# Kernel tuning notes

Hardware: AMD Instinct MI355X
Metric: run time of the kernel (lower is better)

The kernel has to match this reference:

```python
import jax, jax.numpy as jnp
import numpy as np

N = 128000      # total nodes
B = 128         # graphs, 1000 nodes each
L = 4           # max_levels
S_MAX = 1000    # max cluster size (<= PositionalEncoding max_len)
H = 128         # hidden dim (all conv output dims equal)
IN_DIM = 128
OUT_DIM = 1
E = 1024000
TEMP = 0.1


def layer_norm(x, g, b, eps=1e-5):
    mu = jnp.mean(x, axis=-1, keepdims=True)
    v = jnp.mean((x - mu) ** 2, axis=-1, keepdims=True)
    return (x - mu) * jax.lax.rsqrt(v + eps) * g + b


def transformer_conv(x, src, dst, Wq, bq, Wk, bk, Wv, bv, Ws, bs):
    # PyG TransformerConv, heads=1: softmax over in-edges of each dst node
    q = x @ Wq + bq
    k = x @ Wk + bk
    v = x @ Wv + bv
    logits = jnp.sum(q[dst] * k[src], axis=-1) / jnp.sqrt(jnp.float32(q.shape[-1]))
    m = jax.ops.segment_max(logits, dst, num_segments=N)
    e = jnp.exp(logits - m[dst])
    s = jax.ops.segment_sum(e, dst, num_segments=N)
    alpha = e / s[dst]
    agg = jax.ops.segment_sum(alpha[:, None] * v[src], dst, num_segments=N)
    return agg + x @ Ws + bs  # root_weight skip connection


def pos_encoding(S, d):
    pos = jnp.arange(S, dtype=jnp.float32)[:, None]
    div = jnp.exp(jnp.arange(0, d, 2, dtype=jnp.float32) * (-jnp.log(10000.0) / d))
    pe = jnp.zeros((S, d), jnp.float32)
    pe = pe.at[:, 0::2].set(jnp.sin(pos * div))
    pe = pe.at[:, 1::2].set(jnp.cos(pos * div))
    return pe


def gru(xseq, Wih, Whh, bih, bhh):
    # xseq: [G, S, H] -> outputs [G, S, H]; torch GRU gate math
    G = xseq.shape[0]
    def step(h, x_t):
        gi = x_t @ Wih.T + bih
        gh = h @ Whh.T + bhh
        ir, iz, inn = jnp.split(gi, 3, axis=-1)
        hr, hz, hn = jnp.split(gh, 3, axis=-1)
        r = jax.nn.sigmoid(ir + hr)
        z = jax.nn.sigmoid(iz + hz)
        n = jnp.tanh(inn + r * hn)
        h_new = (1.0 - z) * n + z * h
        return h_new, h_new
    h0 = jnp.zeros((G, Whh.shape[1]), xseq.dtype)
    _, outs = jax.lax.scan(step, h0, jnp.swapaxes(xseq, 0, 1))
    return jnp.swapaxes(outs, 0, 1)


def _forward(x, tree_edge_index, call_sequences, batch,
             conv_Wq, conv_bq, conv_Wk, conv_bk, conv_Wv, conv_bv, conv_Ws, conv_bs,
             ln_g, ln_b, centers, proj_W, proj_b,
             gru_Wih, gru_Whh, gru_bih, gru_bhh, seqln_g, seqln_b,
             lin1_W, lin1_b, lin2_W, lin2_b):
    src, dst = tree_edge_index[0], tree_edge_index[1]
    h = x
    for i in range(3):  # conv1/bn1, conv2/bn2, conv4/bn4
        h = transformer_conv(h, src, dst, conv_Wq[i], conv_bq[i], conv_Wk[i],
                             conv_bk[i], conv_Wv[i], conv_bv[i], conv_Ws[i], conv_bs[i])
        h = jax.nn.relu(layer_norm(h, ln_g[i], ln_b[i]))

    # HierarchicalClassifier: cosine-sim soft assignment + center variance loss
    xn = h / jnp.maximum(jnp.linalg.norm(h, axis=-1, keepdims=True), 1e-8)
    cn = centers / jnp.maximum(jnp.linalg.norm(centers, axis=-1, keepdims=True), 1e-8)
    assign = jax.nn.softmax((xn @ cn.T) / TEMP, axis=-1)
    level_ids = jnp.argmax(assign, axis=1).astype(jnp.int32)
    iu0, iu1 = np.triu_indices(L, k=1)
    dvec = jnp.linalg.norm(centers[iu0] - centers[iu1], axis=-1)
    distance = -jnp.var(dvec, ddof=1)  # torch.var is unbiased

    # ragged gather + pad: group nodes by (graph, cluster), sort by call order
    G = B * L
    group = batch * L + level_ids                       # [N]
    order = jnp.argsort(group * N + call_sequences)     # sort by group, then call
    g_sorted = group[order]
    counts = jax.ops.segment_sum(jnp.ones((N,), jnp.int32), group, num_segments=G)
    starts = jnp.cumsum(counts) - counts
    pos = jnp.arange(N, dtype=jnp.int32) - starts[g_sorted]
    seq = jnp.zeros((G, S_MAX, H), h.dtype).at[g_sorted, pos].set(h[order])

    # SequentialRNN: proj -> pos-enc -> GRU -> LayerNorm -> ReLU (mask unused)
    sin = seq @ proj_W + proj_b + pos_encoding(S_MAX, H)[None]
    outs = gru(sin, gru_Wih, gru_Whh, gru_bih, gru_bhh)
    outs = jax.nn.relu(layer_norm(outs, seqln_g, seqln_b))

    # scatter valid positions back; singleton clusters keep raw features
    node_out = jnp.zeros_like(h).at[order].set(outs[g_sorted, pos])
    singleton = (counts[group] == 1)
    gout = jnp.where(singleton[:, None], h, node_out)

    y = jax.nn.gelu(gout @ lin1_W + lin1_b, approximate=False)
    y = jax.nn.sigmoid(y @ lin2_W + lin2_b)
    return y, distance


def setup_inputs():
    key = jax.random.key(0)
    ks = jax.random.split(key, 16)
    p = lambda k, s: jax.random.normal(k, s, jnp.float32) * 0.02
    return {
        "x": jax.random.normal(ks[0], (N, IN_DIM), jnp.float32),
        "tree_edge_index": jax.random.randint(ks[1], (2, E), 0, N, dtype=jnp.int32),
        "call_sequences": jax.random.permutation(ks[2], N).astype(jnp.int32),
        "batch": (jnp.arange(N, dtype=jnp.int32) * B) // N,  # 1000 nodes per graph
        "conv_Wq": p(ks[3], (3, H, H)), "conv_bq": jnp.zeros((3, H), jnp.float32),
        "conv_Wk": p(ks[4], (3, H, H)), "conv_bk": jnp.zeros((3, H), jnp.float32),
        "conv_Wv": p(ks[5], (3, H, H)), "conv_bv": jnp.zeros((3, H), jnp.float32),
        "conv_Ws": p(ks[6], (3, H, H)), "conv_bs": jnp.zeros((3, H), jnp.float32),
        "ln_g": jnp.ones((3, H), jnp.float32), "ln_b": jnp.zeros((3, H), jnp.float32),
        "centers": jax.random.normal(ks[7], (L, H), jnp.float32),
        "proj_W": p(ks[8], (H, H)), "proj_b": jnp.zeros((H,), jnp.float32),
        "gru_Wih": p(ks[9], (3 * H, H)), "gru_Whh": p(ks[10], (3 * H, H)),
        "gru_bih": jnp.zeros((3 * H,), jnp.float32), "gru_bhh": jnp.zeros((3 * H,), jnp.float32),
        "seqln_g": jnp.ones((H,), jnp.float32), "seqln_b": jnp.zeros((H,), jnp.float32),
        "lin1_W": p(ks[11], (H, 8)), "lin1_b": jnp.zeros((8,), jnp.float32),
        "lin2_W": p(ks[12], (8, OUT_DIM)), "lin2_b": jnp.zeros((OUT_DIM,), jnp.float32),
    }


def reference(x, tree_edge_index, call_sequences, batch,
              conv_Wq, conv_bq, conv_Wk, conv_bk, conv_Wv, conv_bv, conv_Ws, conv_bs,
              ln_g, ln_b, centers, proj_W, proj_b,
              gru_Wih, gru_Whh, gru_bih, gru_bhh, seqln_g, seqln_b,
              lin1_W, lin1_b, lin2_W, lin2_b):
    return _forward(x, tree_edge_index, call_sequences, batch,
                    conv_Wq, conv_bq, conv_Wk, conv_bk, conv_Wv, conv_bv, conv_Ws, conv_bs,
                    ln_g, ln_b, centers, proj_W, proj_b,
                    gru_Wih, gru_Whh, gru_bih, gru_bhh, seqln_g, seqln_b,
                    lin1_W, lin1_b, lin2_W, lin2_b)
```

## Files before the change

### kernel.cpp

```cpp
#include <hip/hip_runtime.h>

#define NN 128000
#define EE 1024000
#define HH 128
#define GG 512
#define SMAX 1000
#define NCHUNK 500

typedef unsigned int u32;
typedef unsigned short u16;

constexpr size_t NH     = (size_t)NN*HH;
constexpr size_t F_H    = 0;
constexpr size_t F_A    = NH;
constexpr size_t F_B    = 2*NH;
constexpr size_t F_NODE = F_A + (size_t)NN*192;
constexpr size_t F_CN   = 3*NH;
constexpr size_t F_WKT  = F_CN   + 512;
constexpr size_t F_WQK  = F_WKT  + 3*16384;
constexpr size_t F_BQK  = F_WQK  + 3*16384;
constexpr size_t F_CW   = F_BQK  + 3*128;
constexpr size_t F_PEW  = F_CW   + 128*384;
constexpr size_t F_PEB  = F_PEW  + 1000*384;
constexpr size_t F_END  = F_PEB  + 1000*128;

constexpr size_t I_ROWP = 0;
constexpr size_t I_CUR  = I_ROWP + NN + 8;
constexpr size_t I_COL  = I_CUR  + NN;
constexpr size_t I_GRP  = I_COL  + EE;
constexpr size_t I_INV  = I_GRP  + NN;
constexpr size_t I_POS  = I_INV  + NN;
constexpr size_t I_GN   = I_POS  + NN;
constexpr size_t I_CNT  = I_GN   + (size_t)GG*SMAX;
constexpr size_t I_CH   = I_CNT  + GG;
constexpr size_t I_BS   = I_CH   + (size_t)NCHUNK*GG;
constexpr size_t I_WT   = I_BS   + 512;
constexpr size_t I_END  = I_WT   + 64*384;

constexpr size_t WS_NEEDED = F_END*4 + I_END*4;

__device__ inline float wredf(float v){
  #pragma unroll
  for (int o = 32; o; o >>= 1) v += __shfl_xor(v, o);
  return v;
}
__device__ inline u32 bf16rne(float f){
  u32 u = __float_as_uint(f);
  return (u + 0x7fffu + ((u >> 16) & 1u)) >> 16;
}
__device__ inline float bf2f(u16 u){
  return __uint_as_float(((u32)u) << 16);
}
__device__ inline float frcp(float x){
#if __has_builtin(__builtin_amdgcn_rcpf)
  return __builtin_amdgcn_rcpf(x);
#else
  return 1.f / x;
#endif
}

typedef _Float16 h2_t __attribute__((ext_vector_type(2)));
__device__ inline float dot2f(u32 w, u32 h, float acc){
#if __has_builtin(__builtin_amdgcn_fdot2)
  return __builtin_amdgcn_fdot2(__builtin_bit_cast(h2_t, w),
                                __builtin_bit_cast(h2_t, h), acc, false);
#else
  float r;
  asm("v_dot2_f32_f16 %0, %1, %2, %3" : "=v"(r) : "v"(w), "v"(h), "v"(acc));
  return r;
#endif
}
#define PIN4(v) asm volatile("" : "+v"((v).x), "+v"((v).y), "+v"((v).z), "+v"((v).w))

__global__ void k_sentinel(float* __restrict__ out, int n, float val){
  int i = blockIdx.x * 256 + threadIdx.x;
  if (i < n) out[i] = val;
}

__global__ void k_zero(int* __restrict__ p){
  p[blockIdx.x * 256 + threadIdx.x] = 0;
}
__global__ void k_hist(const int* __restrict__ dst, int* __restrict__ deg){
  int e = blockIdx.x * 256 + threadIdx.x;
  atomicAdd(&deg[dst[e]], 1);
}
__global__ void k_s1(const int* __restrict__ deg, int* __restrict__ bsum){
  __shared__ int red[256];
  int t = threadIdx.x;
  red[t] = deg[blockIdx.x * 256 + t];
  __syncthreads();
  for (int s = 128; s; s >>= 1){ if (t < s) red[t] += red[t + s]; __syncthreads(); }
  if (!t) bsum[blockIdx.x] = red[0];
}
__global__ void k_s2(int* __restrict__ bsum){
  __shared__ int arr[512];
  int t = threadIdx.x;
  int v0 = (t < NCHUNK) ? bsum[t] : 0;
  arr[t] = v0; __syncthreads();
  for (int off = 1; off < 512; off <<= 1){
    int v = (t >= off) ? arr[t - off] : 0;
    __syncthreads();
    arr[t] += v;
    __syncthreads();
  }
  if (t < NCHUNK) bsum[t] = arr[t] - v0;
}
__global__ void k_s3(const int* __restrict__ bsum, int* __restrict__ row_ptr,
                     int* __restrict__ cursor){
  __shared__ int arr[256];
  int t = threadIdx.x;
  int i = blockIdx.x * 256 + t;
  int v0 = cursor[i];
  arr[t] = v0; __syncthreads();
  for (int off = 1; off < 256; off <<= 1){
    int v = (t >= off) ? arr[t - off] : 0;
    __syncthreads();
    arr[t] += v;
    __syncthreads();
  }
  int exc = arr[t] - v0 + bsum[blockIdx.x];
  row_ptr[i] = exc;
  cursor[i]  = exc;
  if (i == 0) row_ptr[NN] = EE;
}
__global__ void k_scatter(const int* __restrict__ src, const int* __restrict__ dst,
                          int* __restrict__ cursor, int* __restrict__ col){
  int e = blockIdx.x * 256 + threadIdx.x;
  int idx = atomicAdd(&cursor[dst[e]], 1);
  col[idx] = src[e];
}

__global__ void k_setup(const float* __restrict__ centers, float* __restrict__ cn,
                        float* __restrict__ dist_out){
  __shared__ float red[128];
  int t = threadIdx.x;
  for (int l = 0; l < 4; ++l){
    float v = centers[l*128 + t];
    red[t] = v * v; __syncthreads();
    for (int s = 64; s; s >>= 1){ if (t < s) red[t] += red[t + s]; __syncthreads(); }
    float nrm = sqrtf(red[0]);
    __syncthreads();
    cn[l*128 + t] = v / fmaxf(nrm, 1e-8f);
  }
  const int iu0[6] = {0,0,0,1,1,2}, iu1[6] = {1,2,3,2,3,3};
  __shared__ float dv[6];
  for (int p = 0; p < 6; ++p){
    float d = centers[iu0[p]*128 + t] - centers[iu1[p]*128 + t];
    red[t] = d * d; __syncthreads();
    for (int s = 64; s; s >>= 1){ if (t < s) red[t] += red[t + s]; __syncthreads(); }
    if (!t) dv[p] = sqrtf(red[0]);
    __syncthreads();
  }
  if (!t){
    float mean = 0.f;
    for (int p = 0; p < 6; ++p) mean += dv[p];
    mean /= 6.f;
    float var = 0.f;
    for (int p = 0; p < 6; ++p){ float d = dv[p] - mean; var += d * d; }
    var /= 5.f;
    dist_out[0] = -var;
  }
}

__global__ void k_pe(const float* __restrict__ projb, float* __restrict__ peb){
  int p = blockIdx.x, t = threadIdx.x;
  float ex  = (float)(t >> 1) * (-2.0f * 9.210340371976184f / 128.0f);
  float ang = (float)p * expf(ex);
  float v = (t & 1) ? cosf(ang) : sinf(ang);
  peb[p*128 + t] = v + projb[t];
}
__global__ void k_pew(const float* __restrict__ peb, const float* __restrict__ Wih,
                      const float* __restrict__ bih, float* __restrict__ pew){
  int p = blockIdx.x;
  int j = blockIdx.y * 128 + threadIdx.x;
  const float* pb = peb + p*128;
  const float* wr = Wih + (size_t)j*128;
  float acc = bih[j];
  #pragma unroll 4
  for (int m = 0; m < 128; ++m) acc += pb[m] * wr[m];
  pew[(size_t)p*384 + j] = acc;
}
__global__ void k_combw(const float* __restrict__ projW, const float* __restrict__ Wih,
                        float* __restrict__ cw){
  int kk = blockIdx.x;
  int j  = blockIdx.y * 128 + threadIdx.x;
  const float* pr = projW + (size_t)kk*128;
  const float* wr = Wih + (size_t)j*128;
  float acc = 0.f;
  #pragma unroll 4
  for (int m = 0; m < 128; ++m) acc += pr[m] * wr[m];
  cw[(size_t)kk*384 + j] = acc;
}
__global__ void k_tr(const float* __restrict__ Wk, float* __restrict__ wkt){
  int kk = blockIdx.x, l = blockIdx.y, c = threadIdx.x;
  wkt[(size_t)l*16384 + kk*128 + c] = Wk[(size_t)l*16384 + c*128 + kk];
}
__global__ void k_mv(const float* __restrict__ M, const float* __restrict__ v,
                     float* __restrict__ out){
  int l = blockIdx.x, i = threadIdx.x;
  const float* row = M + (size_t)l*16384 + (size_t)i*128;
  const float* vv = v + l*128;
  float acc = 0.f;
  #pragma unroll 4
  for (int j = 0; j < 128; ++j) acc += row[j] * vv[j];
  out[l*128 + i] = acc;
}
__global__ void k_packwhh16(const float* __restrict__ Whh, u32* __restrict__ wt){
  int kp = blockIdx.x;
  int j  = blockIdx.y * 128 + threadIdx.x;
  _Float16 a = (_Float16)Whh[(size_t)j*128 + 2*kp];
  _Float16 b = (_Float16)Whh[(size_t)j*128 + 2*kp + 1];
  u32 lo = (u32)__builtin_bit_cast(u16, a);
  u32 hi = (u32)__builtin_bit_cast(u16, b);
  wt[(size_t)j*64 + kp] = (hi << 16) | lo;
}

__global__ __launch_bounds__(256, 2) void k_gemm(
    const float* __restrict__ X, const float* __restrict__ W, int ldw,
    const float* __restrict__ X2, const float* __restrict__ W2,
    const float* __restrict__ bias, const float* __restrict__ pew,
    const int* __restrict__ pos, float* __restrict__ out,
    u16* __restrict__ outb, int ldo,
    const float* __restrict__ lng, const float* __restrict__ lnb,
    const float* __restrict__ bvv, const int* __restrict__ rowp){
  __shared__ __align__(16) float Wl[64*132];
  __shared__ __align__(16) float Xl[64*132];
  int tid = threadIdx.x;
  int rb = blockIdx.x * 128;
  int cb = blockIdx.y * 128;
  int rg = tid >> 4;
  int cg = tid & 15;
  int kxor = (cg >> 2) & 3;
  float acc[8][8];
  #pragma unroll
  for (int a = 0; a < 8; ++a)
    #pragma unroll
    for (int b = 0; b < 8; ++b) acc[a][b] = 0.f;
  int nhalf = X2 ? 4 : 2;
  for (int half = 0; half < nhalf; ++half){
    const float* Xs = (half < 2) ? X : X2;
    const float* Ws = (half < 2) ? W : W2;
    int ldws = (half < 2) ? ldw : 128;
    int hk = half & 1;
    __syncthreads();
    #pragma unroll
    for (int it = 0; it < 8; ++it){
      int idx = it*256 + tid;
      int kk = idx >> 5, c4 = idx & 31;
      *(float4*)&Wl[kk*132 + c4*4] =
          *(const float4*)&Ws[(size_t)(hk*64 + kk)*ldws + cb + c4*4];
    }
    #pragma unroll
    for (int it = 0; it < 8; ++it){
      int idx = it*256 + tid;
      int r = idx >> 4, c4 = idx & 15;
      float4 xv = *(const float4*)&Xs[(size_t)(rb + r)*128 + hk*64 + c4*4];
      Xl[(c4*4+0)*132 + r] = xv.x;
      Xl[(c4*4+1)*132 + r] = xv.y;
      Xl[(c4*4+2)*132 + r] = xv.z;
      Xl[(c4*4+3)*132 + r] = xv.w;
    }
    __syncthreads();
    #pragma unroll 2
    for (int kk = 0; kk < 64; ++kk){
      int kx = kk ^ kxor;
      float4 wa = *(const float4*)&Wl[kx*132 + cg*8];
      float4 wb = *(const float4*)&Wl[kx*132 + cg*8 + 4];
      float4 xa = *(const float4*)&Xl[kx*132 + rg*8];
      float4 xb = *(const float4*)&Xl[kx*132 + rg*8 + 4];
      float xs[8] = {xa.x, xa.y, xa.z, xa.w, xb.x, xb.y, xb.z, xb.w};
      float ws[8] = {wa.x, wa.y, wa.z, wa.w, wb.x, wb.y, wb.z, wb.w};
      #pragma unroll
      for (int rr = 0; rr < 8; ++rr)
        #pragma unroll
        for (int j = 0; j < 8; ++j) acc[rr][j] += xs[rr] * ws[j];
    }
  }
  if (lng){
    float gv[8], bl[8], bb[8], vv[8];
    #pragma unroll
    for (int j = 0; j < 8; ++j){
      int c = cg*8 + j;
      gv[j] = lng[c]; bl[j] = lnb[c]; bb[j] = bias[c]; vv[j] = bvv[c];
    }
    #pragma unroll
    for (int rr = 0; rr < 8; ++rr){
      int r = rb + rg*8 + rr;
      bool deg = rowp[r+1] > rowp[r];
      float rs = 0.f, rq = 0.f;
      #pragma unroll
      for (int j = 0; j < 8; ++j){
        float v = acc[rr][j] + bb[j] + (deg ? vv[j] : 0.f);
        acc[rr][j] = v;
        rs += v; rq += v*v;
      }
      #pragma unroll
      for (int o = 8; o; o >>= 1){ rs += __shfl_xor(rs, o); rq += __shfl_xor(rq, o); }
      float mu = rs * 0.0078125f;
      float var = rq * 0.0078125f - mu*mu;
      float rstd = rsqrtf(var + 1e-5f);
      float ov[8];
      #pragma unroll
      for (int j = 0; j < 8; ++j)
        ov[j] = fmaxf((acc[rr][j] - mu)*rstd*gv[j] + bl[j], 0.f);
      float* op = out + (size_t)r*128 + cg*8;
      *(float4*)op       = *(const float4*)&ov[0];
      *(float4*)(op + 4) = *(const float4*)&ov[4];
    }
    return;
  }
  #pragma unroll
  for (int rr = 0; rr < 8; ++rr){
    int r = rb + rg*8 + rr;
    float bv[8];
    if (pos){
      const float* pw = pew + (size_t)pos[r]*384 + cb + cg*8;
      #pragma unroll
      for (int j = 0; j < 8; ++j) bv[j] = pw[j];
    } else if (bias){
      #pragma unroll
      for (int j = 0; j < 8; ++j) bv[j] = bias[cb + cg*8 + j];
    } else {
      #pragma unroll
      for (int j = 0; j < 8; ++j) bv[j] = 0.f;
    }
    if (outb){
      u16 ob[8];
      #pragma unroll
      for (int j = 0; j < 8; ++j) ob[j] = (u16)bf16rne(acc[rr][j] + bv[j]);
      *(uint4*)(outb + (size_t)r*ldo + cb + cg*8) = *(const uint4*)ob;
    } else {
      float ov[8];
      #pragma unroll
      for (int j = 0; j < 8; ++j) ov[j] = acc[rr][j] + bv[j];
      float* op = out + (size_t)r*ldo + cb + cg*8;
      *(float4*)op       = *(const float4*)&ov[0];
      *(float4*)(op + 4) = *(const float4*)&ov[4];
    }
  }
}

__global__ __launch_bounds__(256) void k_edge(
    const float* __restrict__ qt, const float* __restrict__ xsrc,
    const int* __restrict__ row_ptr, const int* __restrict__ col,
    float* __restrict__ xagg){
  int d = blockIdx.x * 8 + (threadIdx.x >> 5);
  int lane = threadIdx.x & 31;
  int e0 = row_ptr[d], e1 = row_ptr[d+1];
  if (e0 == e1){
    *(float4*)&xagg[(size_t)d*128 + lane*4] = make_float4(0.f, 0.f, 0.f, 0.f);
    return;
  }
  const float S = 0.08838834764831845f;
  float4 qv = *(const float4*)&qt[(size_t)d*128 + lane*4];
  float ss0 = 0.f, ss1 = 0.f;
  float4 A0 = make_float4(0.f,0.f,0.f,0.f), A1 = make_float4(0.f,0.f,0.f,0.f);
  int e = e0;
  for (; e + 1 < e1; e += 2){
    float4 x0 = *(const float4*)&xsrc[(size_t)col[e]  *128 + lane*4];
    float4 x1 = *(const float4*)&xsrc[(size_t)col[e+1]*128 + lane*4];
    float p0 = qv.x*x0.x + qv.y*x0.y + qv.z*x0.z + qv.w*x0.w;
    float p1 = qv.x*x1.x + qv.y*x1.y + qv.z*x1.z + qv.w*x1.w;
    #pragma unroll
    for (int o = 16; o; o >>= 1){ p0 += __shfl_xor(p0, o); p1 += __shfl_xor(p1, o); }
    float el0 = __expf(p0 * S);
    float el1 = __expf(p1 * S);
    ss0 += el0; ss1 += el1;
    A0.x += el0*x0.x; A0.y += el0*x0.y; A0.z += el0*x0.z; A0.w += el0*x0.w;
    A1.x += el1*x1.x; A1.y += el1*x1.y; A1.z += el1*x1.z; A1.w += el1*x1.w;
  }
  if (e < e1){
    float4 x0 = *(const float4*)&xsrc[(size_t)col[e]*128 + lane*4];
    float p0 = qv.x*x0.x + qv.y*x0.y + qv.z*x0.z + qv.w*x0.w;
    #pragma unroll
    for (int o = 16; o; o >>= 1) p0 += __shfl_xor(p0, o);
    float el0 = __expf(p0 * S);
    ss0 += el0;
    A0.x += el0*x0.x; A0.y += el0*x0.y; A0.z += el0*x0.z; A0.w += el0*x0.w;
  }
  float inv = 1.f / (ss0 + ss1);
  *(float4*)&xagg[(size_t)d*128 + lane*4] =
      make_float4((A0.x+A1.x)*inv, (A0.y+A1.y)*inv, (A0.z+A1.z)*inv, (A0.w+A1.w)*inv);
}

__global__ __launch_bounds__(256) void k_lnrelu_cls(
    const float* __restrict__ in, const float* __restrict__ g,
    const float* __restrict__ b, const float* __restrict__ bvv,
    const int* __restrict__ rowp, float* __restrict__ outp,
    const float* __restrict__ cn, const int* __restrict__ batch,
    const int* __restrict__ callsq, int* __restrict__ grp, int* __restrict__ inv){
  int node = blockIdx.x * 4 + (threadIdx.x >> 6);
  int lane = threadIdx.x & 63;
  float x0 = in[(size_t)node*128 + 2*lane], x1 = in[(size_t)node*128 + 2*lane + 1];
  if (rowp[node+1] > rowp[node]){
    x0 += bvv[2*lane];
    x1 += bvv[2*lane + 1];
  }
  float s = wredf(x0 + x1);
  float qq = wredf(x0*x0 + x1*x1);
  float mu = s * 0.0078125f;
  float var = qq * 0.0078125f - mu*mu;
  float rstd = rsqrtf(var + 1e-5f);
  float y0 = fmaxf((x0 - mu)*rstd*g[2*lane]   + b[2*lane],   0.f);
  float y1 = fmaxf((x1 - mu)*rstd*g[2*lane+1] + b[2*lane+1], 0.f);
  outp[(size_t)node*128 + 2*lane]     = y0;
  outp[(size_t)node*128 + 2*lane + 1] = y1;
  float p0 = y0*cn[      2*lane] + y1*cn[      2*lane+1];
  float p1 = y0*cn[128 + 2*lane] + y1*cn[128 + 2*lane+1];
  float p2 = y0*cn[256 + 2*lane] + y1*cn[256 + 2*lane+1];
  float p3 = y0*cn[384 + 2*lane] + y1*cn[384 + 2*lane+1];
  p0 = wredf(p0); p1 = wredf(p1); p2 = wredf(p2); p3 = wredf(p3);
  if (lane == 0){
    float best = p0; int bi = 0;
    if (p1 > best){ best = p1; bi = 1; }
    if (p2 > best){ best = p2; bi = 2; }
    if (p3 > best){ best = p3; bi = 3; }
    grp[node] = batch[node]*4 + bi;
    inv[callsq[node]] = node;
  }
}

__global__ __launch_bounds__(256) void k_g1(const int* __restrict__ inv,
                                            const int* __restrict__ grp,
                                            int* __restrict__ ch){
  __shared__ int hist[GG];
  int c = blockIdx.x, t = threadIdx.x;
  hist[t] = 0; hist[t + 256] = 0;
  __syncthreads();
  int g = grp[inv[c*256 + t]];
  atomicAdd(&hist[g], 1);
  __syncthreads();
  ch[c*GG + t] = hist[t];
  ch[c*GG + 256 + t] = hist[256 + t];
}
__global__ void k_g2(int* __restrict__ ch, int* __restrict__ cnt){
  __shared__ int arr[512];
  int g = blockIdx.x, t = threadIdx.x;
  int v0 = (t < NCHUNK) ? ch[(size_t)t*GG + g] : 0;
  arr[t] = v0; __syncthreads();
  for (int off = 1; off < 512; off <<= 1){
    int v = (t >= off) ? arr[t - off] : 0;
    __syncthreads();
    arr[t] += v;
    __syncthreads();
  }
  if (t < NCHUNK) ch[(size_t)t*GG + g] = arr[t] - v0;
  if (t == 511) cnt[g] = arr[511];
}
__global__ __launch_bounds__(256) void k_g3(
    const int* __restrict__ inv, const int* __restrict__ grp,
    const int* __restrict__ ch, int* __restrict__ pos, int* __restrict__ gn){
  __shared__ int hist[GG];
  int c = blockIdx.x, t = threadIdx.x;
  hist[t] = 0; hist[t + 256] = 0;
  __syncthreads();
  int node = inv[c*256 + t];
  int g = grp[node];
  int lane = t & 63, w = t >> 6;
  int before = 0, total = 0;
  for (int j = 0; j < 64; ++j){
    int gj = __shfl(g, j);
    if (gj == g){ total++; if (j < lane) before++; }
  }
  int base = 0;
  for (int wv = 0; wv < 4; ++wv){
    if (w == wv){
      base = hist[g];
      if (before == total - 1) hist[g] = base + total;
    }
    __syncthreads();
  }
  int p = ch[c*GG + g] + base + before;
  pos[node] = p;
  gn[(size_t)g*SMAX + p] = node;
}

__global__ __launch_bounds__(256)
__attribute__((amdgpu_waves_per_eu(2, 2)))
void k_gru(
    const u16* __restrict__ gi, const u32* __restrict__ wt,
    const float* __restrict__ bhh, const int* __restrict__ gn,
    const int* __restrict__ cnt, u16* __restrict__ node_out){
  __shared__ __align__(16) u16 hb16[2][128];
  int t = threadIdx.x;
  int j = t >> 1;
  int kh = t & 1;
  int g = blockIdx.x;
  int my = cnt[g];
  if (my <= 1) return;
  uint4 wr_[8], wz_[8], wn_[8];
  {
    const uint4* wt4 = (const uint4*)wt;
    size_t b0 = (size_t)(0*128 + j)*16 + kh*8;
    size_t b1 = (size_t)(1*128 + j)*16 + kh*8;
    size_t b2 = (size_t)(2*128 + j)*16 + kh*8;
    #pragma unroll
    for (int s = 0; s < 8; ++s){
      wr_[s] = wt4[b0 + s];
      wz_[s] = wt4[b1 + s];
      wn_[s] = wt4[b2 + s];
    }
    #pragma unroll
    for (int s = 0; s < 8; ++s){
      PIN4(wr_[s]); PIN4(wz_[s]); PIN4(wn_[s]);
    }
  }
  if (t < 128) hb16[0][t] = 0;
  float br = bhh[j], bz = bhh[128 + j], bn = bhh[256 + j];
  const int* gnr = gn + (size_t)g*SMAX;
  float hprev = 0.f;
  int nA = gnr[0];
  int nB = gnr[min(1, my - 1)];
  int nC = gnr[min(2, my - 1)];
  const u16* gA = gi + (size_t)nA*384;
  const u16* gB = gi + (size_t)nB*384;
  const u16* gC = gi + (size_t)nC*384;
  float axr = bf2f(gA[j]), axz = bf2f(gA[128 + j]), axn = bf2f(gA[256 + j]);
  float bxr = bf2f(gB[j]), bxz = bf2f(gB[128 + j]), bxn = bf2f(gB[256 + j]);
  float cxr = bf2f(gC[j]), cxz = bf2f(gC[128 + j]), cxn = bf2f(gC[256 + j]);
  __syncthreads();
  for (int p = 0; p < my; ++p){
    int cur = p & 1, nxt = cur ^ 1;
    float xr = axr, xz = axz, xn = axn;
    int node = nA;
    axr = bxr; axz = bxz; axn = bxn; nA = nB;
    bxr = cxr; bxz = cxz; bxn = cxn; nB = nC;
    nC = gnr[min(p + 3, my - 1)];
    const u16* gN = gi + (size_t)nC*384;
    cxr = bf2f(gN[j]); cxz = bf2f(gN[128 + j]); cxn = bf2f(gN[256 + j]);
    const uint4* HB = (const uint4*)&hb16[cur][0];
    uint4 hh[8];
    #pragma unroll
    for (int s = 0; s < 8; ++s) hh[s] = HB[kh*8 + s];
    __builtin_amdgcn_s_setprio(1);
    float ar = 0.f, az = 0.f, an = 0.f;
    #pragma unroll
    for (int s = 0; s < 8; ++s){
      ar = dot2f(wr_[s].x, hh[s].x, ar); az = dot2f(wz_[s].x, hh[s].x, az); an = dot2f(wn_[s].x, hh[s].x, an);
      ar = dot2f(wr_[s].y, hh[s].y, ar); az = dot2f(wz_[s].y, hh[s].y, az); an = dot2f(wn_[s].y, hh[s].y, an);
      ar = dot2f(wr_[s].z, hh[s].z, ar); az = dot2f(wz_[s].z, hh[s].z, az); an = dot2f(wn_[s].z, hh[s].z, an);
      ar = dot2f(wr_[s].w, hh[s].w, ar); az = dot2f(wz_[s].w, hh[s].w, az); an = dot2f(wn_[s].w, hh[s].w, an);
    }
    ar += __shfl_xor(ar, 1); az += __shfl_xor(az, 1); an += __shfl_xor(an, 1);
    ar += br; az += bz; an += bn;
    float er = __expf(-(xr + ar));
    float r  = frcp(1.f + er);
    float ez = __expf(-(xz + az));
    float z  = frcp(1.f + ez);
    float y  = xn + r * an;
    float e2 = __expf(-2.f * y);
    float n  = (1.f - e2) * frcp(1.f + e2);
    float hnew = n + z * (hprev - n);
    __builtin_amdgcn_s_setprio(0);
    hprev = hnew;
    if (!kh){
      _Float16 hf = (_Float16)hnew;
      hb16[nxt][j] = __builtin_bit_cast(u16, hf);
      node_out[(size_t)node*128 + j] = (u16)bf16rne(hnew);
    }
    asm volatile("s_waitcnt lgkmcnt(0)" ::: "memory");
    __builtin_amdgcn_s_barrier();
    asm volatile("" ::: "memory");
  }
}

__global__ __launch_bounds__(256) void k_head(
    const float* __restrict__ h, const u16* __restrict__ node_out,
    const int* __restrict__ grp, const int* __restrict__ cnt,
    const float* __restrict__ sqg, const float* __restrict__ sqb,
    const float* __restrict__ l1W, const float* __restrict__ l1b,
    const float* __restrict__ l2W, const float* __restrict__ l2b,
    float* __restrict__ out){
  int node = blockIdx.x * 4 + (threadIdx.x >> 6);
  int lane = threadIdx.x & 63;
  bool single = (cnt[grp[node]] == 1);
  float x0, x1;
  if (single){
    x0 = h[(size_t)node*128 + 2*lane];
    x1 = h[(size_t)node*128 + 2*lane + 1];
  } else {
    float r0 = bf2f(node_out[(size_t)node*128 + 2*lane]);
    float r1 = bf2f(node_out[(size_t)node*128 + 2*lane + 1]);
    float s = wredf(r0 + r1);
    float qq = wredf(r0*r0 + r1*r1);
    float mu = s * 0.0078125f;
    float var = qq * 0.0078125f - mu*mu;
    float rstd = rsqrtf(var + 1e-5f);
    x0 = fmaxf((r0 - mu)*rstd*sqg[2*lane]   + sqb[2*lane],   0.f);
    x1 = fmaxf((r1 - mu)*rstd*sqg[2*lane+1] + sqb[2*lane+1], 0.f);
  }
  float acc[8];
  #pragma unroll
  for (int j = 0; j < 8; ++j)
    acc[j] = x0 * l1W[(2*lane)*8 + j] + x1 * l1W[(2*lane + 1)*8 + j];
  #pragma unroll
  for (int o = 32; o; o >>= 1)
    #pragma unroll
    for (int j = 0; j < 8; ++j) acc[j] += __shfl_xor(acc[j], o);
  if (lane == 0){
    float zz = l2b[0];
    #pragma unroll
    for (int j = 0; j < 8; ++j){
      float xx = acc[j] + l1b[j];
      float ge = 0.5f * xx * (1.f + erff(xx * 0.7071067811865476f));
      zz += ge * l2W[j];
    }
    out[node] = 1.f / (1.f + expf(-zz));
  }
}

extern "C" void kernel_launch(void* const* d_in, const int* in_sizes, int n_in,
                              void* d_out, int out_size, void* d_ws, size_t ws_size,
                              hipStream_t stream){
  float* out = (float*)d_out;

  if (ws_size < WS_NEEDED){
    float code = -(float)(ws_size >> 20);
    k_sentinel<<<(out_size + 255)/256, 256, 0, stream>>>(out, out_size, code);
    return;
  }

  const float* x       = (const float*)d_in[0];
  const int*   tei     = (const int*)d_in[1];
  const int*   callsq  = (const int*)d_in[2];
  const int*   batch   = (const int*)d_in[3];
  const float* Wq      = (const float*)d_in[4];
  const float* bq      = (const float*)d_in[5];
  const float* Wk      = (const float*)d_in[6];
  const float* bk      = (const float*)d_in[7];
  const float* Wv      = (const float*)d_in[8];
  const float* bv      = (const float*)d_in[9];
  const float* Wsk     = (const float*)d_in[10];
  const float* bsk     = (const float*)d_in[11];
  const float* lng     = (const float*)d_in[12];
  const float* lnb     = (const float*)d_in[13];
  const float* centers = (const float*)d_in[14];
  const float* projW   = (const float*)d_in[15];
  const float* projb   = (const float*)d_in[16];
  const float* Wih     = (const float*)d_in[17];
  const float* Whh     = (const float*)d_in[18];
  const float* bih     = (const float*)d_in[19];
  const float* bhh     = (const float*)d_in[20];
  const float* sqg     = (const float*)d_in[21];
  const float* sqb     = (const float*)d_in[22];
  const float* l1W     = (const float*)d_in[23];
  const float* l1b     = (const float*)d_in[24];
  const float* l2W     = (const float*)d_in[25];
  const float* l2b     = (const float*)d_in[26];

  float* wf = (float*)d_ws;
  float* f_h    = wf + F_H;
  float* f_a    = wf + F_A;
  float* f_b    = wf + F_B;
  float* f_cn   = wf + F_CN;
  float* f_wkt  = wf + F_WKT;
  float* f_wqk  = wf + F_WQK;
  float* f_bqk  = wf + F_BQK;
  float* f_cw   = wf + F_CW;
  float* f_pew  = wf + F_PEW;
  float* f_peb  = wf + F_PEB;
  u16*   gi_bf  = (u16*)(wf + F_A);
  u16*   no_bf  = (u16*)(wf + F_NODE);
  int* wi = (int*)(wf + F_END);
  int* i_rowp = wi + I_ROWP;
  int* i_cur  = wi + I_CUR;
  int* i_col  = wi + I_COL;
  int* i_grp  = wi + I_GRP;
  int* i_inv  = wi + I_INV;
  int* i_pos  = wi + I_POS;
  int* i_gn   = wi + I_GN;
  int* i_cnt  = wi + I_CNT;
  int* i_ch   = wi + I_CH;
  int* i_bs   = wi + I_BS;
  u32* i_wt   = (u32*)(wi + I_WT);

  const int* esrc = tei;
  const int* edst = tei + EE;

  k_zero<<<NN/256, 256, 0, stream>>>(i_cur);
  k_hist<<<EE/256, 256, 0, stream>>>(edst, i_cur);
  k_s1<<<NCHUNK, 256, 0, stream>>>(i_cur, i_bs);
  k_s2<<<1, 512, 0, stream>>>(i_bs);
  k_s3<<<NCHUNK, 256, 0, stream>>>(i_bs, i_rowp, i_cur);
  k_scatter<<<EE/256, 256, 0, stream>>>(esrc, edst, i_cur, i_col);

  k_setup<<<1, 128, 0, stream>>>(centers, f_cn, out + NN);
  k_pe<<<1000, 128, 0, stream>>>(projb, f_peb);
  k_pew<<<dim3(1000, 3), 128, 0, stream>>>(f_peb, Wih, bih, f_pew);
  k_tr<<<dim3(128, 3), 128, 0, stream>>>(Wk, f_wkt);
  for (int i = 0; i < 3; ++i)
    k_gemm<<<dim3(1, 1), 256, 0, stream>>>(Wq + (size_t)i*16384, f_wkt + (size_t)i*16384,
        128, nullptr, nullptr, nullptr, nullptr, nullptr, f_wqk + (size_t)i*16384,
        nullptr, 128, nullptr, nullptr, nullptr, nullptr);
  k_mv<<<3, 128, 0, stream>>>(Wk, bq, f_bqk);
  k_combw<<<dim3(128, 3), 128, 0, stream>>>(projW, Wih, f_cw);
  k_packwhh16<<<dim3(64, 3), 128, 0, stream>>>(Whh, i_wt);

  for (int i = 0; i < 3; ++i){
    const float* xin = i ? f_h : x;
    size_t wo = (size_t)i * 128 * 128, bo = (size_t)i * 128;
    k_gemm<<<dim3(NN/128, 1), 256, 0, stream>>>(xin, f_wqk + (size_t)i*16384, 128,
        nullptr, nullptr, f_bqk + bo, nullptr, nullptr, f_b, nullptr, 128,
        nullptr, nullptr, nullptr, nullptr);
    k_edge<<<NN/8, 256, 0, stream>>>(f_b, xin, i_rowp, i_col, f_a);
    if (i < 2){
      k_gemm<<<dim3(NN/128, 1), 256, 0, stream>>>(f_a, Wv + wo, 128, xin, Wsk + wo,
          bsk + bo, nullptr, nullptr, f_h, nullptr, 128,
          lng + bo, lnb + bo, bv + bo, i_rowp);
    } else {
      k_gemm<<<dim3(NN/128, 1), 256, 0, stream>>>(f_a, Wv + wo, 128, xin, Wsk + wo,
          bsk + bo, nullptr, nullptr, f_b, nullptr, 128,
          nullptr, nullptr, nullptr, nullptr);
      k_lnrelu_cls<<<NN/4, 256, 0, stream>>>(f_b, lng + bo, lnb + bo, bv + bo, i_rowp,
          f_h, f_cn, batch, callsq, i_grp, i_inv);
    }
  }

  k_g1<<<NCHUNK, 256, 0, stream>>>(i_inv, i_grp, i_ch);
  k_g2<<<GG, 512, 0, stream>>>(i_ch, i_cnt);
  k_g3<<<NCHUNK, 256, 0, stream>>>(i_inv, i_grp, i_ch, i_pos, i_gn);

  k_gemm<<<dim3(NN/128, 3), 256, 0, stream>>>(f_h, f_cw, 384, nullptr, nullptr,
      nullptr, f_pew, i_pos, nullptr, gi_bf, 384, nullptr, nullptr, nullptr, nullptr);

  k_gru<<<GG, 256, 0, stream>>>(gi_bf, i_wt, bhh, i_gn, i_cnt, no_bf);

  k_head<<<NN/4, 256, 0, stream>>>(f_h, no_bf, i_grp, i_cnt, sqg, sqb,
                                   l1W, l1b, l2W, l2b, out);
}
```

Baseline: 2.083 ms.

## Use one thread per hidden unit in GRU recurrence, 128-thread blocks

Restructures the GRU scan kernel from two threads per output unit, each doing half of the dot product plus a shuffle reduction, to a single thread per unit that holds the full 128-wide weight rows in registers. This removes the cross-lane shuffle reduction and halves the threads synchronising at each per-step barrier. Input prefetch depth drops from three steps to one, and output stores are packed into 32-bit writes via a lane shuffle. In exchange, each thread holds twice as many weight registers (192 VGPRs of weights) at one wave per EU, which risks spills or lower latency hiding.

```diff
diff --git a/kernel.cpp b/kernel.cpp
--- a/kernel.cpp
+++ b/kernel.cpp
@@ -475,74 +475,76 @@
   gn[(size_t)g*SMAX + p] = node;
 }
 
-__global__ __launch_bounds__(256)
-__attribute__((amdgpu_waves_per_eu(2, 2)))
+__global__ __launch_bounds__(128)
+__attribute__((amdgpu_waves_per_eu(1, 1)))
 void k_gru(
     const u16* __restrict__ gi, const u32* __restrict__ wt,
     const float* __restrict__ bhh, const int* __restrict__ gn,
     const int* __restrict__ cnt, u16* __restrict__ node_out){
   __shared__ __align__(16) u16 hb16[2][128];
-  int t = threadIdx.x;
-  int j = t >> 1;
-  int kh = t & 1;
+  int j = threadIdx.x;
   int g = blockIdx.x;
   int my = cnt[g];
   if (my <= 1) return;
-  uint4 wr_[8], wz_[8], wn_[8];
+  uint4 wr_[16], wz_[16], wn_[16];
   {
     const uint4* wt4 = (const uint4*)wt;
-    size_t b0 = (size_t)(0*128 + j)*16 + kh*8;
-    size_t b1 = (size_t)(1*128 + j)*16 + kh*8;
-    size_t b2 = (size_t)(2*128 + j)*16 + kh*8;
-    #pragma unroll
-    for (int s = 0; s < 8; ++s){
+    size_t b0 = (size_t)(0*128 + j)*16;
+    size_t b1 = (size_t)(1*128 + j)*16;
+    size_t b2 = (size_t)(2*128 + j)*16;
+    #pragma unroll
+    for (int s = 0; s < 16; ++s){
       wr_[s] = wt4[b0 + s];
       wz_[s] = wt4[b1 + s];
       wn_[s] = wt4[b2 + s];
     }
     #pragma unroll
-    for (int s = 0; s < 8; ++s){
+    for (int s = 0; s < 16; ++s){
       PIN4(wr_[s]); PIN4(wz_[s]); PIN4(wn_[s]);
     }
   }
-  if (t < 128) hb16[0][t] = 0;
+  hb16[0][j] = 0;
   float br = bhh[j], bz = bhh[128 + j], bn = bhh[256 + j];
   const int* gnr = gn + (size_t)g*SMAX;
   float hprev = 0.f;
-  int nA = gnr[0];
-  int nB = gnr[min(1, my - 1)];
-  int nC = gnr[min(2, my - 1)];
-  const u16* gA = gi + (size_t)nA*384;
-  const u16* gB = gi + (size_t)nB*384;
-  const u16* gC = gi + (size_t)nC*384;
-  float axr = bf2f(gA[j]), axz = bf2f(gA[128 + j]), axn = bf2f(gA[256 + j]);
-  float bxr = bf2f(gB[j]), bxz = bf2f(gB[128 + j]), bxn = bf2f(gB[256 + j]);
-  float cxr = bf2f(gC[j]), cxz = bf2f(gC[128 + j]), cxn = bf2f(gC[256 + j]);
+  int node = gnr[0];
+  const u16* g0 = gi + (size_t)node*384;
+  u16 rxr = g0[j], rxz = g0[128 + j], rxn = g0[256 + j];
   __syncthreads();
   for (int p = 0; p < my; ++p){
     int cur = p & 1, nxt = cur ^ 1;
-    float xr = axr, xz = axz, xn = axn;
-    int node = nA;
-    axr = bxr; axz = bxz; axn = bxn; nA = nB;
-    bxr = cxr; bxz = cxz; bxn = cxn; nB = nC;
-    nC = gnr[min(p + 3, my - 1)];
-    const u16* gN = gi + (size_t)nC*384;
-    cxr = bf2f(gN[j]); cxz = bf2f(gN[128 + j]); cxn = bf2f(gN[256 + j]);
+    int nodeN = gnr[min(p + 1, my - 1)];
+    float xr = bf2f(rxr), xz = bf2f(rxz), xn = bf2f(rxn);
+    const u16* gN = gi + (size_t)nodeN*384;
+    rxr = gN[j]; rxz = gN[128 + j]; rxn = gN[256 + j];
     const uint4* HB = (const uint4*)&hb16[cur][0];
-    uint4 hh[8];
-    #pragma unroll
-    for (int s = 0; s < 8; ++s) hh[s] = HB[kh*8 + s];
+    uint4 hh[16];
+    #pragma unroll
+    for (int s = 0; s < 16; ++s) hh[s] = HB[s];
     __builtin_amdgcn_s_setprio(1);
-    float ar = 0.f, az = 0.f, an = 0.f;
-    #pragma unroll
-    for (int s = 0; s < 8; ++s){
-      ar = dot2f(wr_[s].x, hh[s].x, ar); az = dot2f(wz_[s].x, hh[s].x, az); an = dot2f(wn_[s].x, hh[s].x, an);
-      ar = dot2f(wr_[s].y, hh[s].y, ar); az = dot2f(wz_[s].y, hh[s].y, az); an = dot2f(wn_[s].y, hh[s].y, an);
-      ar = dot2f(wr_[s].z, hh[s].z, ar); az = dot2f(wz_[s].z, hh[s].z, az); an = dot2f(wn_[s].z, hh[s].z, an);
-      ar = dot2f(wr_[s].w, hh[s].w, ar); az = dot2f(wz_[s].w, hh[s].w, az); an = dot2f(wn_[s].w, hh[s].w, an);
-    }
-    ar += __shfl_xor(ar, 1); az += __shfl_xor(az, 1); an += __shfl_xor(an, 1);
-    ar += br; az += bz; an += bn;
+    float ar0 = 0.f, ar1 = 0.f, az0 = 0.f, az1 = 0.f, an0 = 0.f, an1 = 0.f;
+    #pragma unroll
+    for (int s = 0; s < 16; s += 2){
+      uint4 h0 = hh[s], h1 = hh[s + 1];
+      uint4 r0 = wr_[s], r1 = wr_[s + 1];
+      uint4 z0 = wz_[s], z1 = wz_[s + 1];
+      uint4 n0 = wn_[s], n1 = wn_[s + 1];
+      ar0 = dot2f(r0.x, h0.x, ar0); ar1 = dot2f(r1.x, h1.x, ar1);
+      az0 = dot2f(z0.x, h0.x, az0); az1 = dot2f(z1.x, h1.x, az1);
+      an0 = dot2f(n0.x, h0.x, an0); an1 = dot2f(n1.x, h1.x, an1);
+      ar0 = dot2f(r0.y, h0.y, ar0); ar1 = dot2f(r1.y, h1.y, ar1);
+      az0 = dot2f(z0.y, h0.y, az0); az1 = dot2f(z1.y, h1.y, az1);
+      an0 = dot2f(n0.y, h0.y, an0); an1 = dot2f(n1.y, h1.y, an1);
+      ar0 = dot2f(r0.z, h0.z, ar0); ar1 = dot2f(r1.z, h1.z, ar1);
+      az0 = dot2f(z0.z, h0.z, az0); az1 = dot2f(z1.z, h1.z, az1);
+      an0 = dot2f(n0.z, h0.z, an0); an1 = dot2f(n1.z, h1.z, an1);
+      ar0 = dot2f(r0.w, h0.w, ar0); ar1 = dot2f(r1.w, h1.w, ar1);
+      az0 = dot2f(z0.w, h0.w, az0); az1 = dot2f(z1.w, h1.w, az1);
+      an0 = dot2f(n0.w, h0.w, an0); an1 = dot2f(n1.w, h1.w, an1);
+    }
+    float ar = ar0 + ar1 + br;
+    float az = az0 + az1 + bz;
+    float an = an0 + an1 + bn;
     float er = __expf(-(xr + ar));
     float r  = frcp(1.f + er);
     float ez = __expf(-(xz + az));
@@ -553,11 +555,13 @@
     float hnew = n + z * (hprev - n);
     __builtin_amdgcn_s_setprio(0);
     hprev = hnew;
-    if (!kh){
-      _Float16 hf = (_Float16)hnew;
-      hb16[nxt][j] = __builtin_bit_cast(u16, hf);
-      node_out[(size_t)node*128 + j] = (u16)bf16rne(hnew);
-    }
+    _Float16 hf = (_Float16)hnew;
+    hb16[nxt][j] = __builtin_bit_cast(u16, hf);
+    u16 hbf = (u16)bf16rne(hnew);
+    u32 pk = ((u32)(u16)__shfl_xor((int)hbf, 1) << 16) | (u32)hbf;
+    if (!(j & 1))
+      *(u32*)(node_out + (size_t)node*128 + j) = pk;
+    node = nodeN;
     asm volatile("s_waitcnt lgkmcnt(0)" ::: "memory");
     __builtin_amdgcn_s_barrier();
     asm volatile("" ::: "memory");
@@ -723,7 +727,7 @@
   k_gemm<<<dim3(NN/128, 3), 256, 0, stream>>>(f_h, f_cw, 384, nullptr, nullptr,
       nullptr, f_pew, i_pos, nullptr, gi_bf, 384, nullptr, nullptr, nullptr, nullptr);
 
-  k_gru<<<GG, 256, 0, stream>>>(gi_bf, i_wt, bhh, i_gn, i_cnt, no_bf);
+  k_gru<<<GG, 128, 0, stream>>>(gi_bf, i_wt, bhh, i_gn, i_cnt, no_bf);
 
   k_head<<<NN/4, 256, 0, stream>>>(f_h, no_bf, i_grp, i_cnt, sqg, sqb,
                                    l1W, l1b, l2W, l2b, out);
```

Measured after the change: 2.100 ms. No clear change (+0.8%).
